# Performance work log

Measured on AMD Instinct MI355X. Metric: run time of the kernel, lower is better.

Reference implementation:

```python
import math
import jax, jax.numpy as jnp
import numpy as np

B, N, M, C, H, POS = 2, 2048, 64, 256, 8, 6
D = C // H  # head_dim = 32
SCALE = 1.0 / math.sqrt(D)
LAMDA = 1.0


def setup_inputs() -> dict:
    key = jax.random.key(0)
    ks = jax.random.split(key, 15)
    s = 0.05
    return {
        "pairwise_g": jax.random.normal(ks[0], (B, N, N, POS), jnp.float32),
        "coset_functions": jax.random.normal(ks[1], (B, N, C), jnp.float32),
        "mask": jnp.ones((B, N), dtype=bool),
        "Wq": jax.random.normal(ks[2], (C, C), jnp.float32) * s,
        "bq": jax.random.normal(ks[3], (C,), jnp.float32) * s,
        "Wk": jax.random.normal(ks[4], (C, C), jnp.float32) * s,
        "bk": jax.random.normal(ks[5], (C,), jnp.float32) * s,
        "Wl": jax.random.normal(ks[6], (C, POS), jnp.float32) * s,
        "bl": jax.random.normal(ks[7], (C,), jnp.float32) * s,
        "u": jax.random.normal(ks[8], (H, D), jnp.float32) * s,
        "v": jax.random.normal(ks[9], (H, D), jnp.float32) * s,
        "Wi": jax.random.normal(ks[10], (C, C), jnp.float32) * s,
        "bi": jax.random.normal(ks[11], (C,), jnp.float32) * s,
        "Wo": jax.random.normal(ks[12], (C, C), jnp.float32) * s,
        "bo": jax.random.normal(ks[13], (C,), jnp.float32) * s,
    }


def reference(pairwise_g, coset_functions, mask, Wq, bq, Wk, bk, Wl, bl, u, v, Wi, bi, Wo, bo):
    # ---- extract_neighbourhoods (mc_samples=M, fill=1.0 -> k == k_ball, permutation irrelevant)
    dists = jnp.linalg.norm(pairwise_g, axis=-1)                      # (B,N,N)
    dists = jnp.where(mask[:, None, :], dists, jnp.float32(1e8))
    _, nbhd_idx = jax.lax.top_k(-dists, M)                            # (B,N,M) nearest neighbors
    nbhd_pg = jnp.take_along_axis(pairwise_g, nbhd_idx[..., None], axis=2)  # (B,N,M,POS)
    gather_rows = jax.vmap(lambda arr, ix: arr[ix])                   # gather along point axis per batch
    nbhd_cf = gather_rows(coset_functions, nbhd_idx)                  # (B,N,M,C)
    nbhd_mask = gather_rows(mask, nbhd_idx)                           # (B,N,M)

    # ---- RelativePositionKernel
    Q = (coset_functions @ Wq.T + bq).reshape(B, N, H, D).transpose(0, 2, 1, 3)  # (B,H,N,D)
    K = (coset_functions @ Wk.T + bk).reshape(B, N, H, D).transpose(0, 2, 1, 3)  # (B,H,N,D)
    e = (nbhd_pg @ Wl.T + bl).reshape(B, N, M, H, D)                  # (B,N,M,H,D)

    S = jnp.einsum('bhnd,bhkd->bhnk', Q, K)                           # dense scores (as original)
    Sg = jnp.take_along_axis(S, nbhd_idx[:, None, :, :], axis=3)      # (B,H,N,M)
    e_term = jnp.einsum('bnmhd,bhnd->bhnm', e, Q + v[None, :, None, :])
    uK = jnp.einsum('hd,bhkd->bhk', u, K)                             # (B,H,N)
    uKg = jnp.take_along_axis(uK[:, :, None, :], nbhd_idx[:, None, :, :], axis=3)  # (B,H,N,M)
    A = (Sg + LAMDA * e_term + uKg) * SCALE
    A = A.transpose(0, 2, 3, 1)                                       # (B,N,M,H)

    # ---- masked softmax over neighbors
    A = jnp.where(nbhd_mask[..., None], A, jnp.float32(-1e38))
    attn = jax.nn.softmax(A, axis=2)                                  # (B,N,M,H)

    # ---- value projection + weighted sum + output linear
    Vv = (nbhd_cf @ Wi.T + bi).reshape(B, N, M, H, D)                 # (B,N,M,H,D)
    out = jnp.einsum('bnmh,bnmhd->bnhd', attn, Vv).reshape(B, N, C)
    out = out @ Wo.T + bo                                             # (B,N,c_out)
    return out
```

## Files before the change

kernel.cpp:

```cpp
#include <hip/hip_runtime.h>
#include <stdint.h>

#define NB 2
#define NN 2048
#define MM 64
#define CC 256
#define HH 8
#define DD 32
#define PP 6
#define ATT_SCALE 0.17677669529663687f
#define NGEMMB 768

typedef __attribute__((ext_vector_type(8))) short short8;
typedef __attribute__((ext_vector_type(4))) float f32x4;

__device__ __forceinline__ uint16_t f2bf(float f) {
  union { float f; uint32_t u; } c; c.f = f;
  return (uint16_t)((c.u + 0x7fffu + ((c.u >> 16) & 1u)) >> 16);
}
__device__ __forceinline__ float blo(uint32_t u) {
  union { uint32_t u; float f; } c; c.u = u << 16; return c.f;
}
__device__ __forceinline__ float bhi(uint32_t u) {
  union { uint32_t u; float f; } c; c.u = u & 0xffff0000u; return c.f;
}

__global__ __launch_bounds__(256) void k_prep(
    const float* __restrict__ cf,
    const float* __restrict__ Wq, const float* __restrict__ Wk,
    const float* __restrict__ Wi, const float* __restrict__ Wo,
    uint16_t* __restrict__ cfb, uint16_t* __restrict__ Wb) {
  const int tid = blockIdx.x * 256 + threadIdx.x;
  const int e0 = tid * 4;
  const int CFN = NB * NN * CC;
  const float* src;
  uint16_t* dst;
  if (e0 < CFN) {
    src = cf + e0; dst = cfb + e0;
  } else {
    const int w = e0 - CFN;
    const int which = w >> 16;
    const int off = w & 65535;
    if (which == 0) src = Wq + off;
    else if (which == 1) src = Wk + off;
    else if (which == 2) src = Wi + off;
    else src = Wo + off;
    dst = Wb + w;
  }
  const float4 x = *(const float4*)src;
  ushort4 o;
  o.x = f2bf(x.x); o.y = f2bf(x.y); o.z = f2bf(x.z); o.w = f2bf(x.w);
  *(ushort4*)dst = o;
}

__global__ __launch_bounds__(256) void k_select_qkv(
    const float* __restrict__ pg,
    const uint16_t* __restrict__ cfb, const uint16_t* __restrict__ Wb,
    const float* __restrict__ bq, const float* __restrict__ bk, const float* __restrict__ bi,
    float* __restrict__ Qo, uint16_t* __restrict__ Ko, uint16_t* __restrict__ Vo,
    int* __restrict__ idx_out, float* __restrict__ npg_out) {
  __shared__ float s_mn[4], s_mx[4];
  __shared__ uint32_t s_wsum[4];
  __shared__ uint32_t s_hist[256];
  __shared__ uint32_t s_scan[256];
  __shared__ float s_cd[NN];
  __shared__ uint16_t s_cj[NN];
  __shared__ int s_tbin;
  __shared__ uint32_t s_c0;
  __shared__ int s_cw;
  __shared__ int s_ct;
  __shared__ int s_idx[MM];

  if (blockIdx.x < NGEMMB) {
    const int task = blockIdx.x * 4 + (threadIdx.x >> 6);
    const int z = task >> 10;
    const int rem = task & 1023;
    const int row0 = (rem & 255) * 16;
    const int c0 = (rem >> 8) * 64;
    const uint16_t* W = Wb + (size_t)z * (CC * CC);
    const float* bias = (z == 0) ? bq : ((z == 1) ? bk : bi);
    const int lane = threadIdx.x & 63;
    const int m = lane & 15;
    const int quad = lane >> 4;

    f32x4 acc0 = {0.f, 0.f, 0.f, 0.f};
    f32x4 acc1 = {0.f, 0.f, 0.f, 0.f};
    f32x4 acc2 = {0.f, 0.f, 0.f, 0.f};
    f32x4 acc3 = {0.f, 0.f, 0.f, 0.f};
#pragma unroll
    for (int k0 = 0; k0 < CC; k0 += 32) {
      const short8 a  = *(const short8*)(cfb + (size_t)(row0 + m) * CC + k0 + quad * 8);
      const short8 f0 = *(const short8*)(W + (size_t)(c0 + 0 + m) * CC + k0 + quad * 8);
      const short8 f1 = *(const short8*)(W + (size_t)(c0 + 16 + m) * CC + k0 + quad * 8);
      const short8 f2 = *(const short8*)(W + (size_t)(c0 + 32 + m) * CC + k0 + quad * 8);
      const short8 f3 = *(const short8*)(W + (size_t)(c0 + 48 + m) * CC + k0 + quad * 8);
      acc0 = __builtin_amdgcn_mfma_f32_16x16x32_bf16(a, f0, acc0, 0, 0, 0);
      acc1 = __builtin_amdgcn_mfma_f32_16x16x32_bf16(a, f1, acc1, 0, 0, 0);
      acc2 = __builtin_amdgcn_mfma_f32_16x16x32_bf16(a, f2, acc2, 0, 0, 0);
      acc3 = __builtin_amdgcn_mfma_f32_16x16x32_bf16(a, f3, acc3, 0, 0, 0);
    }
    const int orow = row0 + quad * 4;
    f32x4 accs[4] = {acc0, acc1, acc2, acc3};
#pragma unroll
    for (int f = 0; f < 4; ++f) {
      const int col = c0 + f * 16 + m;
      const float bv = bias[col];
#pragma unroll
      for (int r = 0; r < 4; ++r) {
        const float val = accs[f][r] + bv;
        const size_t o = (size_t)(orow + r) * CC + col;
        if (z == 0) Qo[o] = val;
        else if (z == 1) Ko[o] = f2bf(val);
        else Vo[o] = f2bf(val);
      }
    }
    return;
  }

  const int row = blockIdx.x - NGEMMB;
  const int t = threadIdx.x;
  const int wave = t >> 6;
  const int lane = t & 63;

  if (t < MM) s_idx[t] = t;

  const float4* base = (const float4*)(pg + (size_t)row * NN * PP);

  float d[8];
  float mn = 3.4e38f, mx = -3.4e38f;
#pragma unroll
  for (int i = 0; i < 4; i++) {
    const int j0 = i * 512 + 2 * t;
    const float4 qa = base[(size_t)(j0 >> 1) * 3 + 0];
    const float4 qb = base[(size_t)(j0 >> 1) * 3 + 1];
    const float4 qc = base[(size_t)(j0 >> 1) * 3 + 2];
    float s0 = __fmul_rn(qa.x, qa.x);
    s0 = __fadd_rn(s0, __fmul_rn(qa.y, qa.y));
    s0 = __fadd_rn(s0, __fmul_rn(qa.z, qa.z));
    s0 = __fadd_rn(s0, __fmul_rn(qa.w, qa.w));
    s0 = __fadd_rn(s0, __fmul_rn(qb.x, qb.x));
    s0 = __fadd_rn(s0, __fmul_rn(qb.y, qb.y));
    float s1 = __fmul_rn(qb.z, qb.z);
    s1 = __fadd_rn(s1, __fmul_rn(qb.w, qb.w));
    s1 = __fadd_rn(s1, __fmul_rn(qc.x, qc.x));
    s1 = __fadd_rn(s1, __fmul_rn(qc.y, qc.y));
    s1 = __fadd_rn(s1, __fmul_rn(qc.z, qc.z));
    s1 = __fadd_rn(s1, __fmul_rn(qc.w, qc.w));
    const float d0 = __fsqrt_rn(s0);
    const float d1 = __fsqrt_rn(s1);
    d[2 * i] = d0; d[2 * i + 1] = d1;
    mn = fminf(mn, fminf(d0, d1));
    mx = fmaxf(mx, fmaxf(d0, d1));
  }

#pragma unroll
  for (int off = 32; off; off >>= 1) {
    mn = fminf(mn, __shfl_xor(mn, off));
    mx = fmaxf(mx, __shfl_xor(mx, off));
  }
  if (lane == 0) { s_mn[wave] = mn; s_mx[wave] = mx; }
  s_hist[t] = 0;
  __syncthreads();
  mn = fminf(fminf(s_mn[0], s_mn[1]), fminf(s_mn[2], s_mn[3]));
  mx = fmaxf(fmaxf(s_mx[0], s_mx[1]), fmaxf(s_mx[2], s_mx[3]));
  const float range = mx - mn;
  const float scale = (range > 0.f) ? (256.0f / range) : 0.f;

  int bins[8];
#pragma unroll
  for (int i = 0; i < 8; i++) {
    int bn = (int)((d[i] - mn) * scale);
    bn = (bn > 255) ? 255 : (bn < 0 ? 0 : bn);
    bins[i] = bn;
    atomicAdd(&s_hist[bn], 1u);
  }
  __syncthreads();

  {
    uint32_t x = s_hist[t];
#pragma unroll
    for (int off = 1; off < 64; off <<= 1) {
      const uint32_t y = __shfl_up(x, off);
      if (lane >= off) x += y;
    }
    if (lane == 63) s_wsum[wave] = x;
    __syncthreads();
    uint32_t pre = 0;
    for (int w = 0; w < wave; w++) pre += s_wsum[w];
    x += pre;
    s_scan[t] = x;
  }
  if (t == 0) { s_cw = 0; s_ct = 0; }
  __syncthreads();

  if (s_scan[t] >= (uint32_t)MM && (t == 0 || s_scan[t - 1] < (uint32_t)MM)) {
    s_tbin = t;
    s_c0 = (t == 0) ? 0u : s_scan[t - 1];
  }
  __syncthreads();

  const int tbin = s_tbin;
  const int c0 = (int)s_c0;

#pragma unroll
  for (int i = 0; i < 8; i++) {
    const int j = (i >> 1) * 512 + 2 * t + (i & 1);
    if (bins[i] < tbin) {
      const int pos = atomicAdd(&s_cw, 1);
      if (pos < MM) s_idx[pos] = j;
    } else if (bins[i] == tbin) {
      const int pos = atomicAdd(&s_ct, 1);
      s_cd[pos] = d[i];
      s_cj[pos] = (uint16_t)j;
    }
  }
  __syncthreads();

  if (t < 64) {
    const int cnt = s_ct;
    const int r = MM - c0;
    for (int it = 0; it < r; ++it) {
      float bd = 3.4e38f; int bj = 0x7fffffff; int bi_ = -1;
      for (int i = t; i < cnt; i += 64) {
        const float dd = s_cd[i]; const int jj = (int)s_cj[i];
        if (dd < bd || (dd == bd && jj < bj)) { bd = dd; bj = jj; bi_ = i; }
      }
#pragma unroll
      for (int off = 32; off; off >>= 1) {
        const float od = __shfl_xor(bd, off);
        const int oj = __shfl_xor(bj, off);
        const int oi = __shfl_xor(bi_, off);
        if (od < bd || (od == bd && oj < bj)) { bd = od; bj = oj; bi_ = oi; }
      }
      if (t == 0 && bi_ >= 0) {
        s_cd[bi_] = 3.4e38f;
        s_idx[c0 + it] = bj;
      }
      __threadfence_block();
    }
  }
  __syncthreads();

  if (t < MM) {
    const int jj = s_idx[t] & (NN - 1);
    idx_out[(size_t)row * MM + t] = jj;
    const float2* p = (const float2*)(pg + ((size_t)row * NN + (size_t)jj) * PP);
    const float2 p0 = p[0], p1 = p[1], p2 = p[2];
    float2* np = (float2*)(npg_out + ((size_t)row * MM + t) * PP);
    np[0] = p0; np[1] = p1; np[2] = p2;
  }
}

__global__ __launch_bounds__(256) void k_attn(
    const float* __restrict__ Q, const uint16_t* __restrict__ K,
    const uint16_t* __restrict__ V,
    const float* __restrict__ Wl, const float* __restrict__ bl,
    const float* __restrict__ u, const float* __restrict__ v,
    const int* __restrict__ idx_in, const float* __restrict__ npg_in,
    uint16_t* __restrict__ attnV) {
  const int row = blockIdx.x;
  const int b = row >> 11;
  const int t = threadIdx.x;
  const int wave = t >> 6;
  const int lane = t & 63;

  __shared__ int s_idx[MM];
  __shared__ float s_npg[MM][7];
  __shared__ float s_qu[CC];
  __shared__ float s_wt[HH][8];
  __shared__ float s_sc[HH][MM];
  __shared__ float s_part[CC];

  const float qv_ = Q[(size_t)row * CC + t];
  s_qu[t] = qv_ + u[t];
  if (t < MM) {
    s_idx[t] = idx_in[(size_t)row * MM + t];
    const float2* np = (const float2*)(npg_in + ((size_t)row * MM + t) * PP);
    const float2 p0 = np[0], p1 = np[1], p2 = np[2];
    s_npg[t][0] = p0.x; s_npg[t][1] = p0.y;
    s_npg[t][2] = p1.x; s_npg[t][3] = p1.y;
    s_npg[t][4] = p2.x; s_npg[t][5] = p2.y;
  }

  {
    const int h = t >> 5;
    const float qpv = qv_ + v[t];
    float part[7];
#pragma unroll
    for (int p = 0; p < 6; p++) part[p] = Wl[(size_t)t * PP + p] * qpv;
    part[6] = bl[t] * qpv;
#pragma unroll
    for (int off = 1; off < 32; off <<= 1) {
#pragma unroll
      for (int p = 0; p < 7; p++) part[p] += __shfl_xor(part[p], off);
    }
    if ((t & 31) == 0) {
#pragma unroll
      for (int p = 0; p < 7; p++) s_wt[h][p] = part[p];
    }
  }
  __syncthreads();

#pragma unroll
  for (int pr = 0; pr < 2; ++pr) {
    const int h = wave + pr * 4;
    const int m = lane;
    const int kidx = s_idx[m] & (NN - 1);
    const uint4* kr = (const uint4*)(K + ((size_t)(b * NN + kidx)) * CC + h * DD);
    float acc = s_wt[h][6];
#pragma unroll
    for (int p = 0; p < 6; p++) acc += s_npg[m][p] * s_wt[h][p];
    const float* qu = &s_qu[h * DD];
    float a2 = 0.f;
#pragma unroll
    for (int w4 = 0; w4 < 4; w4++) {
      const uint4 kv = kr[w4];
      const float* q8 = qu + w4 * 8;
      a2 += q8[0] * blo(kv.x) + q8[1] * bhi(kv.x)
          + q8[2] * blo(kv.y) + q8[3] * bhi(kv.y)
          + q8[4] * blo(kv.z) + q8[5] * bhi(kv.z)
          + q8[6] * blo(kv.w) + q8[7] * bhi(kv.w);
    }
    s_sc[h][m] = (acc + a2) * ATT_SCALE;
  }
  __syncthreads();

#pragma unroll
  for (int pr = 0; pr < 2; ++pr) {
    const int h = wave + pr * 4;
    const float x = s_sc[h][lane];
    float mxv = x;
#pragma unroll
    for (int off = 32; off; off >>= 1) mxv = fmaxf(mxv, __shfl_xor(mxv, off));
    const float e = expf(x - mxv);
    float sm = e;
#pragma unroll
    for (int off = 32; off; off >>= 1) sm += __shfl_xor(sm, off);
    s_sc[h][lane] = e / sm;
  }
  __syncthreads();

  {
    const int h2 = t >> 7;
    const int ci = (t & 127) * 2;
    const int h = ci >> 5;
    const uint32_t* Vb32 = (const uint32_t*)(V + (size_t)b * NN * CC);
    float a0 = 0.f, a1 = 0.f;
#pragma unroll 8
    for (int m = h2; m < MM; m += 2) {
      const uint32_t pv = Vb32[(size_t)(s_idx[m] & (NN - 1)) * (CC / 2) + (ci >> 1)];
      const float p = s_sc[h][m];
      a0 += p * blo(pv);
      a1 += p * bhi(pv);
    }
    if (h2 == 1) { s_part[ci] = a0; s_part[ci + 1] = a1; }
    __syncthreads();
    if (h2 == 0) {
      attnV[(size_t)row * CC + ci]     = f2bf(a0 + s_part[ci]);
      attnV[(size_t)row * CC + ci + 1] = f2bf(a1 + s_part[ci + 1]);
    }
  }
}

__global__ __launch_bounds__(64) void k_gemm_out(const uint16_t* __restrict__ A,
                                                 const uint16_t* __restrict__ W,
                                                 const float* __restrict__ bias,
                                                 float* __restrict__ O) {
  const int lane = threadIdx.x;
  const int m = lane & 15;
  const int quad = lane >> 4;
  const int row0 = blockIdx.x * 16;
  const int c0 = blockIdx.y * 32;

  f32x4 acc0 = {0.f, 0.f, 0.f, 0.f};
  f32x4 acc1 = {0.f, 0.f, 0.f, 0.f};

#pragma unroll
  for (int k0 = 0; k0 < CC; k0 += 32) {
    const short8 a  = *(const short8*)(A + (size_t)(row0 + m) * CC + k0 + quad * 8);
    const short8 f0 = *(const short8*)(W + (size_t)(c0 + 0 + m) * CC + k0 + quad * 8);
    const short8 f1 = *(const short8*)(W + (size_t)(c0 + 16 + m) * CC + k0 + quad * 8);
    acc0 = __builtin_amdgcn_mfma_f32_16x16x32_bf16(a, f0, acc0, 0, 0, 0);
    acc1 = __builtin_amdgcn_mfma_f32_16x16x32_bf16(a, f1, acc1, 0, 0, 0);
  }

  const int orow = row0 + quad * 4;
  f32x4 accs[2] = {acc0, acc1};
#pragma unroll
  for (int f = 0; f < 2; ++f) {
    const int col = c0 + f * 16 + m;
    const float bv = bias[col];
#pragma unroll
    for (int r = 0; r < 4; ++r) {
      O[(size_t)(orow + r) * CC + col] = accs[f][r] + bv;
    }
  }
}

extern "C" void kernel_launch(void* const* d_in, const int* in_sizes, int n_in,
                              void* d_out, int out_size, void* d_ws, size_t ws_size,
                              hipStream_t stream) {
  const float* pg = (const float*)d_in[0];
  const float* cf = (const float*)d_in[1];
  const float* Wq = (const float*)d_in[3];
  const float* bq = (const float*)d_in[4];
  const float* Wk = (const float*)d_in[5];
  const float* bk = (const float*)d_in[6];
  const float* Wl = (const float*)d_in[7];
  const float* bl = (const float*)d_in[8];
  const float* u  = (const float*)d_in[9];
  const float* v  = (const float*)d_in[10];
  const float* Wi = (const float*)d_in[11];
  const float* bi = (const float*)d_in[12];
  const float* Wo = (const float*)d_in[13];
  const float* bo = (const float*)d_in[14];

  char* ws = (char*)d_ws;
  float* Q      = (float*)ws;
  uint16_t* K   = (uint16_t*)(ws + (size_t)4  * (1 << 20));
  uint16_t* V   = (uint16_t*)(ws + (size_t)6  * (1 << 20));
  uint16_t* aV  = (uint16_t*)(ws + (size_t)8  * (1 << 20));
  uint16_t* cfb = (uint16_t*)(ws + (size_t)10 * (1 << 20));
  uint16_t* Wb  = (uint16_t*)(ws + (size_t)12 * (1 << 20));
  int* idxb     = (int*)(ws + (size_t)12 * (1 << 20) + (512 << 10));
  float* npgb   = (float*)(ws + (size_t)13 * (1 << 20) + (512 << 10));
  float* out = (float*)d_out;

  hipLaunchKernelGGL(k_prep, dim3(1280), dim3(256), 0, stream,
                     cf, Wq, Wk, Wi, Wo, cfb, Wb);
  hipLaunchKernelGGL(k_select_qkv, dim3(NGEMMB + NB * NN), dim3(256), 0, stream,
                     pg, cfb, Wb, bq, bk, bi, Q, K, V, idxb, npgb);
  hipLaunchKernelGGL(k_attn, dim3(NB * NN), dim3(256), 0, stream,
                     Q, K, V, Wl, bl, u, v, idxb, npgb, aV);
  hipLaunchKernelGGL(k_gemm_out, dim3(256, 8), dim3(64), 0, stream,
                     aV, Wb + (size_t)3 * CC * CC, bo, out);
}
```

Measured before the change: 356.7 us.

## Replace serial threshold-bin selection with parallel rank sort and reorder blocks

The iterative one-wave argmin loop that picks the remaining neighbours from the threshold bin is replaced by an all-thread rank computation: each candidate counts how many candidates precede it and writes itself directly into its slot. This removes up to 64 serial reduction rounds, each a chain of shuffles and barriers. The threshold-bin search now uses the exclusive prefix from the scan registers, which drops the s_scan shared array and one __syncthreads. Selection blocks are placed before the GEMM blocks in the grid so the longer selection work is scheduled first. The rank loop costs O(cnt^2) work, which could grow large if many distances fall into the threshold bin.

```diff
diff --git a/kernel.cpp b/kernel.cpp
--- a/kernel.cpp
+++ b/kernel.cpp
@@ -10,6 +10,7 @@
 #define PP 6
 #define ATT_SCALE 0.17677669529663687f
 #define NGEMMB 768
+#define NSEL (NB * NN)
 
 typedef __attribute__((ext_vector_type(8))) short short8;
 typedef __attribute__((ext_vector_type(4))) float f32x4;
@@ -62,7 +63,6 @@
   __shared__ float s_mn[4], s_mx[4];
   __shared__ uint32_t s_wsum[4];
   __shared__ uint32_t s_hist[256];
-  __shared__ uint32_t s_scan[256];
   __shared__ float s_cd[NN];
   __shared__ uint16_t s_cj[NN];
   __shared__ int s_tbin;
@@ -71,8 +71,8 @@
   __shared__ int s_ct;
   __shared__ int s_idx[MM];
 
-  if (blockIdx.x < NGEMMB) {
-    const int task = blockIdx.x * 4 + (threadIdx.x >> 6);
+  if (blockIdx.x >= NSEL) {
+    const int task = (blockIdx.x - NSEL) * 4 + (threadIdx.x >> 6);
     const int z = task >> 10;
     const int rem = task & 1023;
     const int row0 = (rem & 255) * 16;
@@ -117,7 +117,7 @@
     return;
   }
 
-  const int row = blockIdx.x - NGEMMB;
+  const int row = blockIdx.x;
   const int t = threadIdx.x;
   const int wave = t >> 6;
   const int lane = t & 63;
@@ -177,25 +177,24 @@
   __syncthreads();
 
   {
-    uint32_t x = s_hist[t];
+    const uint32_t hv = s_hist[t];
+    uint32_t x = hv;
 #pragma unroll
     for (int off = 1; off < 64; off <<= 1) {
       const uint32_t y = __shfl_up(x, off);
       if (lane >= off) x += y;
     }
     if (lane == 63) s_wsum[wave] = x;
+    if (t == 0) { s_cw = 0; s_ct = 0; }
     __syncthreads();
     uint32_t pre = 0;
     for (int w = 0; w < wave; w++) pre += s_wsum[w];
     x += pre;
-    s_scan[t] = x;
-  }
-  if (t == 0) { s_cw = 0; s_ct = 0; }
-  __syncthreads();
-
-  if (s_scan[t] >= (uint32_t)MM && (t == 0 || s_scan[t - 1] < (uint32_t)MM)) {
-    s_tbin = t;
-    s_c0 = (t == 0) ? 0u : s_scan[t - 1];
+    const uint32_t excl = x - hv;
+    if (x >= (uint32_t)MM && excl < (uint32_t)MM) {
+      s_tbin = t;
+      s_c0 = excl;
+    }
   }
   __syncthreads();
 
@@ -216,27 +215,19 @@
   }
   __syncthreads();
 
-  if (t < 64) {
+  {
     const int cnt = s_ct;
     const int r = MM - c0;
-    for (int it = 0; it < r; ++it) {
-      float bd = 3.4e38f; int bj = 0x7fffffff; int bi_ = -1;
-      for (int i = t; i < cnt; i += 64) {
-        const float dd = s_cd[i]; const int jj = (int)s_cj[i];
-        if (dd < bd || (dd == bd && jj < bj)) { bd = dd; bj = jj; bi_ = i; }
+    for (int i = t; i < cnt; i += 256) {
+      const float di = s_cd[i];
+      const int ji = (int)s_cj[i];
+      int rank = 0;
+      for (int k2 = 0; k2 < cnt; k2++) {
+        const float dk = s_cd[k2];
+        const int jk = (int)s_cj[k2];
+        rank += (dk < di || (dk == di && jk < ji)) ? 1 : 0;
       }
-#pragma unroll
-      for (int off = 32; off; off >>= 1) {
-        const float od = __shfl_xor(bd, off);
-        const int oj = __shfl_xor(bj, off);
-        const int oi = __shfl_xor(bi_, off);
-        if (od < bd || (od == bd && oj < bj)) { bd = od; bj = oj; bi_ = oi; }
-      }
-      if (t == 0 && bi_ >= 0) {
-        s_cd[bi_] = 3.4e38f;
-        s_idx[c0 + it] = bj;
-      }
-      __threadfence_block();
+      if (rank < r) s_idx[c0 + rank] = ji;
     }
   }
   __syncthreads();
@@ -428,7 +419,7 @@
 
   hipLaunchKernelGGL(k_prep, dim3(1280), dim3(256), 0, stream,
                      cf, Wq, Wk, Wi, Wo, cfb, Wb);
-  hipLaunchKernelGGL(k_select_qkv, dim3(NGEMMB + NB * NN), dim3(256), 0, stream,
+  hipLaunchKernelGGL(k_select_qkv, dim3(NSEL + NGEMMB), dim3(256), 0, stream,
                      pg, cfb, Wb, bq, bk, bi, Q, K, V, idxb, npgb);
   hipLaunchKernelGGL(k_attn, dim3(NB * NN), dim3(256), 0, stream,
                      Q, K, V, Wl, bl, u, v, idxb, npgb, aV);
```

New measurement: 360.9 us. Within noise of the previous version (+1.2%).
